# Performance work log

Hardware: AMD Instinct MI355X
Metric: run time of the kernel (lower is better)

## Reference

```python
import jax, jax.numpy as jnp
import numpy as np

IN_DIM = 768
ATT_DIM = 512
N_HEADS = 8
HEAD_DIM = ATT_DIM // N_HEADS


def setup_inputs() -> dict:
    key = jax.random.key(0)
    k1, k2, k3 = jax.random.split(key, 3)
    X = jax.random.normal(k1, (4, 2048, IN_DIM), dtype=jnp.float32)
    # qkv linear (no bias): weight [3*att_dim, in_dim], torch convention y = x W^T
    W_qkv = jax.random.normal(k2, (3 * ATT_DIM, IN_DIM), dtype=jnp.float32) * (1.0 / np.sqrt(IN_DIM))
    W_out = jax.random.normal(k3, (IN_DIM, ATT_DIM), dtype=jnp.float32) * (1.0 / np.sqrt(ATT_DIM))
    b_out = jnp.zeros((IN_DIM,), dtype=jnp.float32)
    return {"X": X, "W_qkv": W_qkv, "W_out": W_out, "b_out": b_out}


def reference(X, W_qkv, W_out, b_out):
    b, n, _ = X.shape
    QKV = jnp.einsum('bnf,cf->bnc', X, W_qkv)  # [b, n, 3*att_dim]
    # rearrange 'b n (p h d) -> p b h n d'
    QKV = QKV.reshape(b, n, 3, N_HEADS, HEAD_DIM).transpose(2, 0, 3, 1, 4)
    Q, K, V = QKV[0], QKV[1], QKV[2]  # each [b, h, n, d]
    scores = jnp.einsum('bhid,bhjd->bhij', Q, K) / np.sqrt(HEAD_DIM)
    A = jax.nn.softmax(scores, axis=-1)  # dropout p=0 -> identity
    Y = jnp.einsum('bhij,bhjd->bhid', A, V)
    Y = Y.transpose(0, 2, 1, 3).reshape(b, n, ATT_DIM)  # 'b h n d -> b n (h d)'
    return jnp.einsum('bna,oa->bno', Y, W_out) + b_out
```

## Files before the change

kernel.cpp:

```cpp
#include <hip/hip_runtime.h>

typedef __bf16 bf16;
typedef unsigned int u32;
typedef __attribute__((ext_vector_type(8))) __bf16 bf16x8;
typedef __attribute__((ext_vector_type(4))) __bf16 bf16x4;
typedef __attribute__((ext_vector_type(4))) float floatx4;

#define IN_DIM  768
#define ATT_DIM 512
#define NH      8
#define HD      64
#define BATCH   4
#define SEQ     2048
#define M_TOT   (BATCH*SEQ)
#define QKV_N   (3*ATT_DIM)

#define QSCALE 0.18033688011112042f

__device__ __forceinline__ void cp16(void* lds, const void* g) {
    __builtin_amdgcn_global_load_lds((const __attribute__((address_space(1))) u32*)g,
                                     (__attribute__((address_space(3))) u32*)lds, 16, 0, 0);
}
__device__ __forceinline__ const bf16* swz(const bf16* b, int row, int chunk) {
    return b + row * 64 + (((chunk) ^ (row & 7)) << 3);
}

#define N8_X  (M_TOT * IN_DIM / 8)
#define N8_WQ (QKV_N * IN_DIM / 8)
#define N8_WO (IN_DIM * ATT_DIM / 8)
#define N8_ALL (N8_X + N8_WQ + N8_WO)

__global__ __launch_bounds__(256) void cvt_all(const float* __restrict__ X,
                                               const float* __restrict__ Wq,
                                               const float* __restrict__ Wo,
                                               bf16* __restrict__ Xb,
                                               bf16* __restrict__ Wqb,
                                               bf16* __restrict__ Wob) {
    int i = blockIdx.x * 256 + threadIdx.x;
    const float* s; bf16* d; int off;
    if (i < N8_X)            { s = X;  d = Xb;  off = i; }
    else if (i < N8_X+N8_WQ) { s = Wq; d = Wqb; off = i - N8_X; }
    else                     { s = Wo; d = Wob; off = i - N8_X - N8_WQ; }
    const float4 a = ((const float4*)s)[2*off];
    const float4 b = ((const float4*)s)[2*off+1];
    bf16x8 o = {(bf16)a.x,(bf16)a.y,(bf16)a.z,(bf16)a.w,
                (bf16)b.x,(bf16)b.y,(bf16)b.z,(bf16)b.w};
    ((bf16x8*)d)[off] = o;
}

__global__ __launch_bounds__(256) void qkv_gemm(const bf16* __restrict__ Xb,
                                                const bf16* __restrict__ Wb,
                                                bf16* __restrict__ Q,
                                                bf16* __restrict__ Kv,
                                                bf16* __restrict__ VT) {
    __shared__ __align__(16) char smraw[34816];
    bf16* As = (bf16*)smraw;
    bf16* Bs = (bf16*)(smraw + 16384);

    const int tid  = threadIdx.x;
    const int bm0  = blockIdx.y * 128;
    const int bn0  = blockIdx.x * 128;
    const int wave = tid >> 6, lane = tid & 63;
    const int quad = lane >> 4, l15 = lane & 15;
    const int wm = (wave >> 1) * 64, wn = (wave & 1) * 64;
    const int r8 = lane >> 3, cc = (lane & 7) ^ r8;

    const bf16* ag = Xb + (size_t)(bm0 + wave * 32 + r8) * IN_DIM + cc * 8;
    const bf16* bg = Wb + (size_t)(bn0 + wave * 32 + r8) * IN_DIM + cc * 8;

    floatx4 acc[4][4];
#pragma unroll
    for (int i = 0; i < 4; ++i)
#pragma unroll
        for (int j = 0; j < 4; ++j) acc[i][j] = (floatx4){0.f, 0.f, 0.f, 0.f};

    for (int kt = 0; kt < IN_DIM / 64; ++kt) {
        __syncthreads();
#pragma unroll
        for (int it = 0; it < 4; ++it) {
            cp16(&As[(wave * 32 + it * 8) * 64], ag + it * (8 * IN_DIM) + kt * 64);
            cp16(&Bs[(wave * 32 + it * 8) * 64], bg + it * (8 * IN_DIM) + kt * 64);
        }
        __syncthreads();

        bf16x8 af[2][4], bfr[2][4];
#pragma unroll
        for (int kh = 0; kh < 2; ++kh)
#pragma unroll
            for (int i = 0; i < 4; ++i) {
                af[kh][i]  = *(const bf16x8*)swz(As, wm + i * 16 + l15, kh * 4 + quad);
                bfr[kh][i] = *(const bf16x8*)swz(Bs, wn + i * 16 + l15, kh * 4 + quad);
            }
#pragma unroll
        for (int kh = 0; kh < 2; ++kh)
#pragma unroll
            for (int i = 0; i < 4; ++i)
#pragma unroll
                for (int j = 0; j < 4; ++j)
                    acc[i][j] = __builtin_amdgcn_mfma_f32_16x16x32_bf16(af[kh][i], bfr[kh][j], acc[i][j], 0, 0, 0);
    }

    const int b = bm0 >> 11, nbase = bm0 & 2047;

    if (bn0 < 1024) {
#pragma unroll
        for (int i = 0; i < 4; ++i)
#pragma unroll
            for (int j = 0; j < 4; ++j)
#pragma unroll
                for (int r = 0; r < 4; ++r) {
                    const int row = bm0 + wm + i * 16 + quad * 4 + r;
                    const int col = bn0 + wn + j * 16 + l15;
                    const float v = acc[i][j][r];
                    const int rem = col & 511;
                    const int h = rem >> 6, d = rem & 63;
                    const int n = row & 2047;
                    const size_t idx = (((size_t)((row >> 11) * NH + h)) * SEQ + n) * HD + d;
                    if (col < 512) Q[idx]  = (bf16)(v * QSCALE);
                    else           Kv[idx] = (bf16)v;
                }
    } else {
        __syncthreads();
        bf16 (*Ts)[136] = (bf16(*)[136])smraw;
#pragma unroll
        for (int i = 0; i < 4; ++i)
#pragma unroll
            for (int j = 0; j < 4; ++j) {
                bf16x4 pk = {(bf16)acc[i][j][0], (bf16)acc[i][j][1],
                             (bf16)acc[i][j][2], (bf16)acc[i][j][3]};
                *(bf16x4*)&Ts[wn + j * 16 + l15][wm + i * 16 + quad * 4] = pk;
            }
        __syncthreads();
        const int cb = bn0 - 1024;
#pragma unroll
        for (int t2 = 0; t2 < 8; ++t2) {
            const int id = tid + t2 * 256;
            const int c = id >> 4, nc = (id & 15) * 8;
            const int col = cb + c;
            const int h = col >> 6, d = col & 63;
            *(bf16x8*)&VT[(((size_t)(b * NH + h)) * HD + d) * SEQ + nbase + nc] =
                *(const bf16x8*)&Ts[c][nc];
        }
    }
}

__global__ __launch_bounds__(256, 2) void attn(const bf16* __restrict__ Q,
                                               const bf16* __restrict__ K,
                                               const bf16* __restrict__ VT,
                                               bf16* __restrict__ Y) {
    __shared__ bf16 Ks[2][64 * 64];
    __shared__ bf16 VTs[2][64 * 64];
    __shared__ bf16 Ps[4][2][16 * 64];

    const int tid  = threadIdx.x;
    const int wave = tid >> 6, lane = tid & 63;
    const int quad = lane >> 4, l15 = lane & 15;
    const int bh = blockIdx.x;
    const int q0 = blockIdx.y * 128;
    const bf16* Qg = Q  + (size_t)bh * SEQ * HD;
    const bf16* Kg = K  + (size_t)bh * SEQ * HD;
    const bf16* Vg = VT + (size_t)bh * HD * SEQ;

    const int r8 = lane >> 3, cc = (lane & 7) ^ r8;

    bf16x8 aq[2][2];
#pragma unroll
    for (int g = 0; g < 2; ++g) {
        const size_t qrow = (size_t)(q0 + wave * 32 + g * 16 + l15) * 64;
        aq[g][0] = *(const bf16x8*)&Qg[qrow + quad * 8];
        aq[g][1] = *(const bf16x8*)&Qg[qrow + 32 + quad * 8];
    }

    const bf16* kg0 = Kg + (size_t)(wave * 16 + r8) * 64 + cc * 8;
    const bf16* kg1 = Kg + (size_t)(wave * 16 + 8 + r8) * 64 + cc * 8;
    const bf16* vg0 = Vg + (size_t)(wave * 16 + r8) * 2048 + cc * 8;
    const bf16* vg1 = Vg + (size_t)(wave * 16 + 8 + r8) * 2048 + cc * 8;

    cp16(&Ks[0][(wave * 16) * 64], kg0);
    cp16(&Ks[0][(wave * 16 + 8) * 64], kg1);
    cp16(&VTs[0][(wave * 16) * 64], vg0);
    cp16(&VTs[0][(wave * 16 + 8) * 64], vg1);

    float l[2] = {0.f, 0.f};
    floatx4 o[2][4];
#pragma unroll
    for (int g = 0; g < 2; ++g)
#pragma unroll
        for (int db = 0; db < 4; ++db) o[g][db] = (floatx4){0.f, 0.f, 0.f, 0.f};

    for (int kt = 0; kt < SEQ / 64; ++kt) {
        const int cur = kt & 1, nb = cur ^ 1;
        __syncthreads();
        if (kt < SEQ / 64 - 1) {
            cp16(&Ks[nb][(wave * 16) * 64], kg0 + (size_t)(kt + 1) * 4096);
            cp16(&Ks[nb][(wave * 16 + 8) * 64], kg1 + (size_t)(kt + 1) * 4096);
            cp16(&VTs[nb][(wave * 16) * 64], vg0 + (kt + 1) * 64);
            cp16(&VTs[nb][(wave * 16 + 8) * 64], vg1 + (kt + 1) * 64);
        }

#pragma unroll
        for (int t = 0; t < 4; ++t) {
            const int kr = t * 16 + l15;
            const bf16x8 k0 = *(const bf16x8*)swz(Ks[cur], kr, quad);
            const bf16x8 k1 = *(const bf16x8*)swz(Ks[cur], kr, 4 + quad);
            const int c = t * 2 + (quad >> 1);
            const int poff = l15 * 64 + ((c ^ (l15 & 7)) << 3) + ((quad & 1) << 2);
#pragma unroll
            for (int g = 0; g < 2; ++g) {
                floatx4 z = (floatx4){0.f, 0.f, 0.f, 0.f};
                z = __builtin_amdgcn_mfma_f32_16x16x32_bf16(k0, aq[g][0], z, 0, 0, 0);
                z = __builtin_amdgcn_mfma_f32_16x16x32_bf16(k1, aq[g][1], z, 0, 0, 0);
                const float p0 = __builtin_amdgcn_exp2f(z[0]);
                const float p1 = __builtin_amdgcn_exp2f(z[1]);
                const float p2 = __builtin_amdgcn_exp2f(z[2]);
                const float p3 = __builtin_amdgcn_exp2f(z[3]);
                l[g] += (p0 + p1) + (p2 + p3);
                bf16x4 pk = {(bf16)p0, (bf16)p1, (bf16)p2, (bf16)p3};
                *(bf16x4*)&Ps[wave][g][poff] = pk;
            }
        }
        bf16x8 pa[2][2];
#pragma unroll
        for (int g = 0; g < 2; ++g) {
            pa[g][0] = *(const bf16x8*)swz(&Ps[wave][g][0], l15, quad);
            pa[g][1] = *(const bf16x8*)swz(&Ps[wave][g][0], l15, 4 + quad);
        }

#pragma unroll
        for (int db = 0; db < 4; ++db) {
            const int vr = db * 16 + l15;
            const bf16x8 v0 = *(const bf16x8*)swz(VTs[cur], vr, quad);
            const bf16x8 v1 = *(const bf16x8*)swz(VTs[cur], vr, 4 + quad);
#pragma unroll
            for (int g = 0; g < 2; ++g) {
                o[g][db] = __builtin_amdgcn_mfma_f32_16x16x32_bf16(pa[g][0], v0, o[g][db], 0, 0, 0);
                o[g][db] = __builtin_amdgcn_mfma_f32_16x16x32_bf16(pa[g][1], v1, o[g][db], 0, 0, 0);
            }
        }
    }

    const int b = bh >> 3, h = bh & 7;
#pragma unroll
    for (int g = 0; g < 2; ++g) {
        float lg = l[g];
        lg += __shfl_xor(lg, 16, 64);
        lg += __shfl_xor(lg, 32, 64);
        const float inv = 1.0f / lg;
        float linv[4];
#pragma unroll
        for (int r = 0; r < 4; ++r)
            linv[r] = __int_as_float(__builtin_amdgcn_ds_bpermute((quad * 4 + r) * 4,
                                                                  __float_as_int(inv)));
#pragma unroll
        for (int db = 0; db < 4; ++db)
#pragma unroll
            for (int r = 0; r < 4; ++r) {
                const int n = q0 + wave * 32 + g * 16 + quad * 4 + r;
                Y[((size_t)(b * SEQ + n)) * ATT_DIM + h * HD + db * 16 + l15] =
                    (bf16)(o[g][db][r] * linv[r]);
            }
    }
}

__global__ __launch_bounds__(256) void out_gemm(const bf16* __restrict__ Yb,
                                                const bf16* __restrict__ Wb,
                                                const float* __restrict__ bias,
                                                float* __restrict__ out) {
    __shared__ __align__(16) bf16 As[64 * 64];
    __shared__ __align__(16) bf16 Bs[128 * 64];

    const int tid  = threadIdx.x;
    const int bm0  = blockIdx.y * 64;
    const int bn0  = blockIdx.x * 128;
    const int wave = tid >> 6, lane = tid & 63;
    const int quad = lane >> 4, l15 = lane & 15;
    const int wm = (wave >> 1) * 32, wn = (wave & 1) * 64;
    const int r8 = lane >> 3, cc = (lane & 7) ^ r8;

    const bf16* ag = Yb + (size_t)(bm0 + wave * 16 + r8) * ATT_DIM + cc * 8;
    const bf16* bg = Wb + (size_t)(bn0 + wave * 32 + r8) * ATT_DIM + cc * 8;

    floatx4 acc[2][4];
#pragma unroll
    for (int i = 0; i < 2; ++i)
#pragma unroll
        for (int j = 0; j < 4; ++j) acc[i][j] = (floatx4){0.f, 0.f, 0.f, 0.f};

    for (int kt = 0; kt < ATT_DIM / 64; ++kt) {
        __syncthreads();
#pragma unroll
        for (int it = 0; it < 2; ++it)
            cp16(&As[(wave * 16 + it * 8) * 64], ag + it * (8 * ATT_DIM) + kt * 64);
#pragma unroll
        for (int it = 0; it < 4; ++it)
            cp16(&Bs[(wave * 32 + it * 8) * 64], bg + it * (8 * ATT_DIM) + kt * 64);
        __syncthreads();

#pragma unroll
        for (int kh = 0; kh < 2; ++kh) {
            bf16x8 af[2], bfr[4];
#pragma unroll
            for (int i = 0; i < 2; ++i)
                af[i]  = *(const bf16x8*)swz(As, wm + i * 16 + l15, kh * 4 + quad);
#pragma unroll
            for (int j = 0; j < 4; ++j)
                bfr[j] = *(const bf16x8*)swz(Bs, wn + j * 16 + l15, kh * 4 + quad);
#pragma unroll
            for (int i = 0; i < 2; ++i)
#pragma unroll
                for (int j = 0; j < 4; ++j)
                    acc[i][j] = __builtin_amdgcn_mfma_f32_16x16x32_bf16(af[i], bfr[j], acc[i][j], 0, 0, 0);
        }
    }

#pragma unroll
    for (int i = 0; i < 2; ++i)
#pragma unroll
        for (int j = 0; j < 4; ++j)
#pragma unroll
            for (int r = 0; r < 4; ++r) {
                const int row = bm0 + wm + i * 16 + quad * 4 + r;
                const int col = bn0 + wn + j * 16 + l15;
                out[(size_t)row * IN_DIM + col] = acc[i][j][r] + bias[col];
            }
}

extern "C" void kernel_launch(void* const* d_in, const int* in_sizes, int n_in,
                              void* d_out, int out_size, void* d_ws, size_t ws_size,
                              hipStream_t stream) {
    const float* X    = (const float*)d_in[0];
    const float* Wqkv = (const float*)d_in[1];
    const float* Wout = (const float*)d_in[2];
    const float* bout = (const float*)d_in[3];
    float* out = (float*)d_out;

    char* ws = (char*)d_ws;
    size_t off = 0;
    bf16* Xb  = (bf16*)(ws + off); off += (size_t)M_TOT * IN_DIM * 2;
    bf16* Wqb = (bf16*)(ws + off); off += (size_t)QKV_N * IN_DIM * 2;
    bf16* Wob = (bf16*)(ws + off); off += (size_t)IN_DIM * ATT_DIM * 2;
    const size_t T = (size_t)BATCH * NH * SEQ * HD * 2;
    bf16* Q  = (bf16*)(ws + off); off += T;
    bf16* K  = (bf16*)(ws + off); off += T;
    bf16* VT = (bf16*)(ws + off); off += T;
    bf16* Y  = (bf16*)(ws + off); off += T;

    cvt_all<<<N8_ALL / 256, 256, 0, stream>>>(X, Wqkv, Wout, Xb, Wqb, Wob);
    qkv_gemm<<<dim3(QKV_N / 128, M_TOT / 128), 256, 0, stream>>>(Xb, Wqb, Q, K, VT);
    attn<<<dim3(BATCH * NH, SEQ / 128), 256, 0, stream>>>(Q, K, VT, Y);
    out_gemm<<<dim3(IN_DIM / 128, M_TOT / 64), 256, 0, stream>>>(Y, Wob, bout, out);
}
```

Baseline: 178.5 us.

## Enlarge attention KV tile to 128 and out-GEMM M tile to 128

The attention kernel now stages 128 keys and values per double-buffered iteration, with a 128-wide swizzled VT layout, and processes them in two 64-key halves. This halves the number of block barriers and loop iterations. The output GEMM tile grows from 64x128 to 128x128 with a 4x4 accumulator per wave, raising MFMA work per LDS load. In exchange, LDS use and register pressure go up, which may lower occupancy, and the out_gemm grid is halved.

```diff
diff --git a/kernel.cpp b/kernel.cpp
--- a/kernel.cpp
+++ b/kernel.cpp
@@ -23,6 +23,9 @@
 }
 __device__ __forceinline__ const bf16* swz(const bf16* b, int row, int chunk) {
     return b + row * 64 + (((chunk) ^ (row & 7)) << 3);
+}
+__device__ __forceinline__ const bf16* swz128(const bf16* b, int row, int chunk) {
+    return b + row * 128 + (((chunk) ^ (row & 15)) << 3);
 }
 
 #define N8_X  (M_TOT * IN_DIM / 8)
@@ -148,8 +151,8 @@
                                                const bf16* __restrict__ K,
                                                const bf16* __restrict__ VT,
                                                bf16* __restrict__ Y) {
-    __shared__ bf16 Ks[2][64 * 64];
-    __shared__ bf16 VTs[2][64 * 64];
+    __shared__ bf16 Ks[2][128 * 64];
+    __shared__ bf16 VTs[2][64 * 128];
     __shared__ bf16 Ps[4][2][16 * 64];
 
     const int tid  = threadIdx.x;
@@ -162,6 +165,7 @@
     const bf16* Vg = VT + (size_t)bh * HD * SEQ;
 
     const int r8 = lane >> 3, cc = (lane & 7) ^ r8;
+    const int r4 = lane >> 4;
 
     bf16x8 aq[2][2];
 #pragma unroll
@@ -171,16 +175,7 @@
         aq[g][1] = *(const bf16x8*)&Qg[qrow + 32 + quad * 8];
     }
 
-    const bf16* kg0 = Kg + (size_t)(wave * 16 + r8) * 64 + cc * 8;
-    const bf16* kg1 = Kg + (size_t)(wave * 16 + 8 + r8) * 64 + cc * 8;
-    const bf16* vg0 = Vg + (size_t)(wave * 16 + r8) * 2048 + cc * 8;
-    const bf16* vg1 = Vg + (size_t)(wave * 16 + 8 + r8) * 2048 + cc * 8;
-
-    cp16(&Ks[0][(wave * 16) * 64], kg0);
-    cp16(&Ks[0][(wave * 16 + 8) * 64], kg1);
-    cp16(&VTs[0][(wave * 16) * 64], vg0);
-    cp16(&VTs[0][(wave * 16 + 8) * 64], vg1);
-
+    const bf16* kgw = Kg + (size_t)(wave * 32 + r8) * 64 + cc * 8;
     float l[2] = {0.f, 0.f};
     floatx4 o[2][4];
 #pragma unroll
@@ -188,53 +183,73 @@
 #pragma unroll
         for (int db = 0; db < 4; ++db) o[g][db] = (floatx4){0.f, 0.f, 0.f, 0.f};
 
-    for (int kt = 0; kt < SEQ / 64; ++kt) {
+#pragma unroll
+    for (int it = 0; it < 4; ++it)
+        cp16(&Ks[0][(wave * 32 + it * 8) * 64], kgw + (size_t)it * 8 * 64);
+#pragma unroll
+    for (int it = 0; it < 4; ++it) {
+        const int vrow = wave * 16 + it * 4 + r4;
+        const int vcc = (lane & 15) ^ (vrow & 15);
+        cp16(&VTs[0][(wave * 16 + it * 4) * 128],
+             Vg + (size_t)vrow * 2048 + vcc * 8);
+    }
+
+    for (int kt = 0; kt < SEQ / 128; ++kt) {
         const int cur = kt & 1, nb = cur ^ 1;
         __syncthreads();
-        if (kt < SEQ / 64 - 1) {
-            cp16(&Ks[nb][(wave * 16) * 64], kg0 + (size_t)(kt + 1) * 4096);
-            cp16(&Ks[nb][(wave * 16 + 8) * 64], kg1 + (size_t)(kt + 1) * 4096);
-            cp16(&VTs[nb][(wave * 16) * 64], vg0 + (kt + 1) * 64);
-            cp16(&VTs[nb][(wave * 16 + 8) * 64], vg1 + (kt + 1) * 64);
-        }
-
-#pragma unroll
-        for (int t = 0; t < 4; ++t) {
-            const int kr = t * 16 + l15;
-            const bf16x8 k0 = *(const bf16x8*)swz(Ks[cur], kr, quad);
-            const bf16x8 k1 = *(const bf16x8*)swz(Ks[cur], kr, 4 + quad);
-            const int c = t * 2 + (quad >> 1);
-            const int poff = l15 * 64 + ((c ^ (l15 & 7)) << 3) + ((quad & 1) << 2);
+        if (kt < SEQ / 128 - 1) {
+#pragma unroll
+            for (int it = 0; it < 4; ++it)
+                cp16(&Ks[nb][(wave * 32 + it * 8) * 64],
+                     kgw + (size_t)(kt + 1) * 128 * 64 + (size_t)it * 8 * 64);
+#pragma unroll
+            for (int it = 0; it < 4; ++it) {
+                const int vrow = wave * 16 + it * 4 + r4;
+                const int vcc = (lane & 15) ^ (vrow & 15);
+                cp16(&VTs[nb][(wave * 16 + it * 4) * 128],
+                     Vg + (size_t)vrow * 2048 + (kt + 1) * 128 + vcc * 8);
+            }
+        }
+
+#pragma unroll
+        for (int s = 0; s < 2; ++s) {
+#pragma unroll
+            for (int t = 0; t < 4; ++t) {
+                const int kr = s * 64 + t * 16 + l15;
+                const bf16x8 k0 = *(const bf16x8*)swz(Ks[cur], kr, quad);
+                const bf16x8 k1 = *(const bf16x8*)swz(Ks[cur], kr, 4 + quad);
+                const int c = t * 2 + (quad >> 1);
+                const int poff = l15 * 64 + ((c ^ (l15 & 7)) << 3) + ((quad & 1) << 2);
+#pragma unroll
+                for (int g = 0; g < 2; ++g) {
+                    floatx4 z = (floatx4){0.f, 0.f, 0.f, 0.f};
+                    z = __builtin_amdgcn_mfma_f32_16x16x32_bf16(k0, aq[g][0], z, 0, 0, 0);
+                    z = __builtin_amdgcn_mfma_f32_16x16x32_bf16(k1, aq[g][1], z, 0, 0, 0);
+                    const float p0 = __builtin_amdgcn_exp2f(z[0]);
+                    const float p1 = __builtin_amdgcn_exp2f(z[1]);
+                    const float p2 = __builtin_amdgcn_exp2f(z[2]);
+                    const float p3 = __builtin_amdgcn_exp2f(z[3]);
+                    l[g] += (p0 + p1) + (p2 + p3);
+                    bf16x4 pk = {(bf16)p0, (bf16)p1, (bf16)p2, (bf16)p3};
+                    *(bf16x4*)&Ps[wave][g][poff] = pk;
+                }
+            }
+            bf16x8 pa[2][2];
 #pragma unroll
             for (int g = 0; g < 2; ++g) {
-                floatx4 z = (floatx4){0.f, 0.f, 0.f, 0.f};
-                z = __builtin_amdgcn_mfma_f32_16x16x32_bf16(k0, aq[g][0], z, 0, 0, 0);
-                z = __builtin_amdgcn_mfma_f32_16x16x32_bf16(k1, aq[g][1], z, 0, 0, 0);
-                const float p0 = __builtin_amdgcn_exp2f(z[0]);
-                const float p1 = __builtin_amdgcn_exp2f(z[1]);
-                const float p2 = __builtin_amdgcn_exp2f(z[2]);
-                const float p3 = __builtin_amdgcn_exp2f(z[3]);
-                l[g] += (p0 + p1) + (p2 + p3);
-                bf16x4 pk = {(bf16)p0, (bf16)p1, (bf16)p2, (bf16)p3};
-                *(bf16x4*)&Ps[wave][g][poff] = pk;
-            }
-        }
-        bf16x8 pa[2][2];
-#pragma unroll
-        for (int g = 0; g < 2; ++g) {
-            pa[g][0] = *(const bf16x8*)swz(&Ps[wave][g][0], l15, quad);
-            pa[g][1] = *(const bf16x8*)swz(&Ps[wave][g][0], l15, 4 + quad);
-        }
-
-#pragma unroll
-        for (int db = 0; db < 4; ++db) {
-            const int vr = db * 16 + l15;
-            const bf16x8 v0 = *(const bf16x8*)swz(VTs[cur], vr, quad);
-            const bf16x8 v1 = *(const bf16x8*)swz(VTs[cur], vr, 4 + quad);
-#pragma unroll
-            for (int g = 0; g < 2; ++g) {
-                o[g][db] = __builtin_amdgcn_mfma_f32_16x16x32_bf16(pa[g][0], v0, o[g][db], 0, 0, 0);
-                o[g][db] = __builtin_amdgcn_mfma_f32_16x16x32_bf16(pa[g][1], v1, o[g][db], 0, 0, 0);
+                pa[g][0] = *(const bf16x8*)swz(&Ps[wave][g][0], l15, quad);
+                pa[g][1] = *(const bf16x8*)swz(&Ps[wave][g][0], l15, 4 + quad);
+            }
+#pragma unroll
+            for (int db = 0; db < 4; ++db) {
+                const int vr = db * 16 + l15;
+                const bf16x8 v0 = *(const bf16x8*)swz128(VTs[cur], vr, s * 8 + quad);
+                const bf16x8 v1 = *(const bf16x8*)swz128(VTs[cur], vr, s * 8 + 4 + quad);
+#pragma unroll
+                for (int g = 0; g < 2; ++g) {
+                    o[g][db] = __builtin_amdgcn_mfma_f32_16x16x32_bf16(pa[g][0], v0, o[g][db], 0, 0, 0);
+                    o[g][db] = __builtin_amdgcn_mfma_f32_16x16x32_bf16(pa[g][1], v1, o[g][db], 0, 0, 0);
+                }
             }
         }
     }
@@ -266,55 +281,54 @@
                                                 const bf16* __restrict__ Wb,
                                                 const float* __restrict__ bias,
                                                 float* __restrict__ out) {
-    __shared__ __align__(16) bf16 As[64 * 64];
+    __shared__ __align__(16) bf16 As[128 * 64];
     __shared__ __align__(16) bf16 Bs[128 * 64];
 
     const int tid  = threadIdx.x;
-    const int bm0  = blockIdx.y * 64;
+    const int bm0  = blockIdx.y * 128;
     const int bn0  = blockIdx.x * 128;
     const int wave = tid >> 6, lane = tid & 63;
     const int quad = lane >> 4, l15 = lane & 15;
-    const int wm = (wave >> 1) * 32, wn = (wave & 1) * 64;
+    const int wm = (wave >> 1) * 64, wn = (wave & 1) * 64;
     const int r8 = lane >> 3, cc = (lane & 7) ^ r8;
 
-    const bf16* ag = Yb + (size_t)(bm0 + wave * 16 + r8) * ATT_DIM + cc * 8;
+    const bf16* ag = Yb + (size_t)(bm0 + wave * 32 + r8) * ATT_DIM + cc * 8;
     const bf16* bg = Wb + (size_t)(bn0 + wave * 32 + r8) * ATT_DIM + cc * 8;
 
-    floatx4 acc[2][4];
-#pragma unroll
-    for (int i = 0; i < 2; ++i)
+    floatx4 acc[4][4];
+#pragma unroll
+    for (int i = 0; i < 4; ++i)
 #pragma unroll
         for (int j = 0; j < 4; ++j) acc[i][j] = (floatx4){0.f, 0.f, 0.f, 0.f};
 
     for (int kt = 0; kt < ATT_DIM / 64; ++kt) {
         __syncthreads();
 #pragma unroll
-        for (int it = 0; it < 2; ++it)
-            cp16(&As[(wave * 16 + it * 8) * 64], ag + it * (8 * ATT_DIM) + kt * 64);
-#pragma unroll
-        for (int it = 0; it < 4; ++it)
+        for (int it = 0; it < 4; ++it) {
+            cp16(&As[(wave * 32 + it * 8) * 64], ag + it * (8 * ATT_DIM) + kt * 64);
             cp16(&Bs[(wave * 32 + it * 8) * 64], bg + it * (8 * ATT_DIM) + kt * 64);
-        __syncthreads();
-
-#pragma unroll
-        for (int kh = 0; kh < 2; ++kh) {
-            bf16x8 af[2], bfr[4];
-#pragma unroll
-            for (int i = 0; i < 2; ++i)
-                af[i]  = *(const bf16x8*)swz(As, wm + i * 16 + l15, kh * 4 + quad);
-#pragma unroll
-            for (int j = 0; j < 4; ++j)
-                bfr[j] = *(const bf16x8*)swz(Bs, wn + j * 16 + l15, kh * 4 + quad);
-#pragma unroll
-            for (int i = 0; i < 2; ++i)
+        }
+        __syncthreads();
+
+        bf16x8 af[2][4], bfr[2][4];
+#pragma unroll
+        for (int kh = 0; kh < 2; ++kh)
+#pragma unroll
+            for (int i = 0; i < 4; ++i) {
+                af[kh][i]  = *(const bf16x8*)swz(As, wm + i * 16 + l15, kh * 4 + quad);
+                bfr[kh][i] = *(const bf16x8*)swz(Bs, wn + i * 16 + l15, kh * 4 + quad);
+            }
+#pragma unroll
+        for (int kh = 0; kh < 2; ++kh)
+#pragma unroll
+            for (int i = 0; i < 4; ++i)
 #pragma unroll
                 for (int j = 0; j < 4; ++j)
-                    acc[i][j] = __builtin_amdgcn_mfma_f32_16x16x32_bf16(af[i], bfr[j], acc[i][j], 0, 0, 0);
-        }
-    }
-
-#pragma unroll
-    for (int i = 0; i < 2; ++i)
+                    acc[i][j] = __builtin_amdgcn_mfma_f32_16x16x32_bf16(af[kh][i], bfr[kh][j], acc[i][j], 0, 0, 0);
+    }
+
+#pragma unroll
+    for (int i = 0; i < 4; ++i)
 #pragma unroll
         for (int j = 0; j < 4; ++j)
 #pragma unroll
@@ -348,5 +362,5 @@
     cvt_all<<<N8_ALL / 256, 256, 0, stream>>>(X, Wqkv, Wout, Xb, Wqb, Wob);
     qkv_gemm<<<dim3(QKV_N / 128, M_TOT / 128), 256, 0, stream>>>(Xb, Wqb, Q, K, VT);
     attn<<<dim3(BATCH * NH, SEQ / 128), 256, 0, stream>>>(Q, K, VT, Y);
-    out_gemm<<<dim3(IN_DIM / 128, M_TOT / 64), 256, 0, stream>>>(Y, Wob, bout, out);
-}
+    out_gemm<<<dim3(IN_DIM / 128, M_TOT / 128), 256, 0, stream>>>(Y, Wob, bout, out);
+}
```

Measured after the change: 160.1 us. 10.3% less time.
